# Optimization experiments

Measured on AMD Instinct MI355X. Metric: run time of the kernel, lower is better.

Reference implementation:

```python
import jax, jax.numpy as jnp
import numpy as np

N_NODES = 50000
N_EDGES = 600000
D = 128
R = 8
EPS = 1e-5


def layer_norm(x, g, b):
    mu = jnp.mean(x, axis=-1, keepdims=True)
    var = jnp.mean(jnp.square(x - mu), axis=-1, keepdims=True)
    return (x - mu) * jax.lax.rsqrt(var + EPS) * g + b


def rgcn(x, src, dst, edge_attr, W, root, bias, num_nodes):
    # x: [N, d], W: [R, d, f], edge_attr: [E, R] soft relation weights
    E = src.shape[0]
    f = W.shape[-1]
    msg = jnp.zeros((E, f), dtype=x.dtype)
    for r in range(W.shape[0]):  # small fixed relation count
        hr = x @ W[r]                       # [N, f]
        msg = msg + hr[src] * edge_attr[:, r][:, None]  # gather + weight
    agg = jax.ops.segment_sum(msg, dst, num_segments=num_nodes)  # scatter-add
    return agg + x @ root + bias


def setup_inputs() -> dict:
    key = jax.random.key(0)
    ks = jax.random.split(key, 12)
    s = 1.0 / np.sqrt(D)
    return {
        "x": jax.random.normal(ks[0], (N_NODES, D), dtype=jnp.float32),
        "edge_index": jax.random.randint(ks[1], (2, N_EDGES), 0, N_NODES, dtype=jnp.int64),
        "edge_attr": jax.random.uniform(ks[2], (N_EDGES, R), dtype=jnp.float32),
        "ln1_g": jnp.ones((D,), jnp.float32),
        "ln1_b": jnp.zeros((D,), jnp.float32),
        "W1": jax.random.normal(ks[3], (R, D, D), jnp.float32) * s,
        "root1": jax.random.normal(ks[4], (D, D), jnp.float32) * s,
        "b1": jnp.zeros((D,), jnp.float32),
        "ln2_g": jnp.ones((D,), jnp.float32),
        "ln2_b": jnp.zeros((D,), jnp.float32),
        "W2": jax.random.normal(ks[5], (R, D, D), jnp.float32) * s,
        "root2": jax.random.normal(ks[6], (D, D), jnp.float32) * s,
        "b2": jnp.zeros((D,), jnp.float32),
    }


def reference(x, edge_index, edge_attr, ln1_g, ln1_b, W1, root1, b1,
              ln2_g, ln2_b, W2, root2, b2):
    src, dst = edge_index[0], edge_index[1]
    identity = x
    out = jax.nn.gelu(layer_norm(x, ln1_g, ln1_b), approximate=False)
    out = rgcn(out, src, dst, edge_attr, W1, root1, b1, x.shape[0])
    out = jax.nn.gelu(layer_norm(out, ln2_g, ln2_b), approximate=False)
    out = rgcn(out, src, dst, edge_attr, W2, root2, b2, x.shape[0])
    return out + identity
```

## Files before the change

### kernel.cpp

```cpp
#include <hip/hip_runtime.h>
#include <hip/hip_bf16.h>

typedef __attribute__((ext_vector_type(8))) short short8;
typedef __attribute__((ext_vector_type(4))) float f32x4;

#define LDA 1152

__device__ __forceinline__ float bf2f(unsigned short u) {
    union { unsigned int i; float f; } v; v.i = ((unsigned int)u) << 16; return v.f;
}
__device__ __forceinline__ unsigned short f2bf(float f) {
    __hip_bfloat16 h = __float2bfloat16(f);
    union { __hip_bfloat16 h; unsigned short u; } v; v.h = h; return v.u;
}
__device__ __forceinline__ float gelu_exact(float t) {
    return 0.5f * t * (1.0f + erff(t * 0.70710678118654752f));
}

__global__ void prep_w(const float* __restrict__ W1, const float* __restrict__ root1,
                       unsigned short* __restrict__ Bf1,
                       const float* __restrict__ W2, const float* __restrict__ root2,
                       unsigned short* __restrict__ Bf2) {
    int i = blockIdx.x * 256 + threadIdx.x;
    const float* W = W1; const float* root = root1; unsigned short* Bfrag = Bf1;
    if (i >= 1152 * 128) {
        i -= 1152 * 128; W = W2; root = root2; Bfrag = Bf2;
        if (i >= 1152 * 128) return;
    }
    int kp = i >> 7, n = i & 127;
    float v;
    if (kp < 1024) {
        int d = kp >> 3, r = kp & 7;
        v = W[((size_t)r * 128 + d) * 128 + n];
    } else {
        v = root[(size_t)(kp - 1024) * 128 + n];
    }
    int kb = kp >> 5;
    int lane = (((kp >> 3) & 3) << 4) | (n & 15);
    int j = kp & 7;
    int t = n >> 4;
    Bfrag[(((size_t)(kb * 8 + t) * 64 + lane) << 3) + j] = f2bf(v);
}

__global__ void zero_i32(int* __restrict__ p, int n) {
    int i = blockIdx.x * 256 + threadIdx.x;
    if (i < n) p[i] = 0;
}

__global__ void hist_dst(const int* __restrict__ ei, int* __restrict__ cnt, int E) {
    int e = blockIdx.x * 256 + threadIdx.x;
    if (e >= E) return;
    atomicAdd(&cnt[ei[E + e]], 1);
}

__global__ void scan1(const int* __restrict__ cnt, int* __restrict__ part,
                      int* __restrict__ bsum, int N) {
    int i = blockIdx.x * 256 + threadIdx.x;
    int v = (i < N) ? cnt[i] : 0;
    int lane = threadIdx.x & 63, wid = threadIdx.x >> 6;
    int s = v;
    #pragma unroll
    for (int off = 1; off < 64; off <<= 1) {
        int t = __shfl_up(s, off);
        if (lane >= off) s += t;
    }
    __shared__ int wsum[4];
    if (lane == 63) wsum[wid] = s;
    __syncthreads();
    int add = 0;
    for (int w = 0; w < wid; ++w) add += wsum[w];
    s += add;
    part[i] = s - v;
    if (threadIdx.x == 255) bsum[blockIdx.x] = s;
}

__global__ void scan2(int* __restrict__ bsum, int nb) {
    int i = threadIdx.x;
    int v = (i < nb) ? bsum[i] : 0;
    int lane = threadIdx.x & 63, wid = threadIdx.x >> 6;
    int s = v;
    #pragma unroll
    for (int off = 1; off < 64; off <<= 1) {
        int t = __shfl_up(s, off);
        if (lane >= off) s += t;
    }
    __shared__ int wsum[4];
    if (lane == 63) wsum[wid] = s;
    __syncthreads();
    int add = 0;
    for (int w = 0; w < wid; ++w) add += wsum[w];
    s += add;
    if (i < nb) bsum[i] = s - v;
}

__global__ void scan3(const int* __restrict__ part, const int* __restrict__ bsum,
                      int* __restrict__ rowptr, int* __restrict__ woff, int N) {
    int i = blockIdx.x * 256 + threadIdx.x;
    if (i >= N) return;
    int v = part[i] + bsum[blockIdx.x];
    rowptr[i] = v;
    woff[i] = v;
}

__global__ void scatter_edges(const int* __restrict__ ei, const float4* __restrict__ attr,
                              int* __restrict__ woff, int* __restrict__ esrc,
                              float4* __restrict__ eattr, int E) {
    int e = blockIdx.x * 256 + threadIdx.x;
    if (e >= E) return;
    int src = ei[e], dst = ei[E + e];
    int p = atomicAdd(&woff[dst], 1);
    esrc[p] = src;
    eattr[2 * p]     = attr[2 * e];
    eattr[2 * p + 1] = attr[2 * e + 1];
}

__global__ void ln_gelu(const float* __restrict__ x, const float* __restrict__ g,
                        const float* __restrict__ b, unsigned short* __restrict__ A, int N) {
    int row = (blockIdx.x * blockDim.x + threadIdx.x) >> 6;
    if (row >= N) return;
    int lane = threadIdx.x & 63;
    float2 v = *(const float2*)(x + (size_t)row * 128 + lane * 2);
    float s = v.x + v.y;
    #pragma unroll
    for (int o = 32; o; o >>= 1) s += __shfl_xor(s, o);
    float mu = s * (1.0f / 128.0f);
    float d0 = v.x - mu, d1 = v.y - mu;
    float q = d0 * d0 + d1 * d1;
    #pragma unroll
    for (int o = 32; o; o >>= 1) q += __shfl_xor(q, o);
    float rs = rsqrtf(q * (1.0f / 128.0f) + 1e-5f);
    float2 gg = *(const float2*)(g + lane * 2);
    float2 bb = *(const float2*)(b + lane * 2);
    ushort2 o2;
    o2.x = f2bf(gelu_exact(d0 * rs * gg.x + bb.x));
    o2.y = f2bf(gelu_exact(d1 * rs * gg.y + bb.y));
    *(ushort2*)(A + (size_t)row * LDA + 1024 + lane * 2) = o2;
}

__global__ __launch_bounds__(256) void edge_z(const int* __restrict__ rowptr,
                                              const int* __restrict__ esrc,
                                              const float4* __restrict__ eattr,
                                              unsigned short* __restrict__ A, int N, int E) {
    int row = (blockIdx.x << 2) + (threadIdx.x >> 6);
    if (row >= N) return;
    int lane = threadIdx.x & 63;
    int e0 = rowptr[row];
    int e1 = (row + 1 < N) ? rowptr[row + 1] : E;
    float a0[8] = {0,0,0,0,0,0,0,0};
    float a1[8] = {0,0,0,0,0,0,0,0};
    const unsigned short* yl = A + 1024 + lane * 2;

    #define EDGE_FMA(hv, W0, W1) do {                                  \
        float y0 = bf2f((unsigned short)((hv) & 0xffffu));             \
        float y1 = bf2f((unsigned short)((hv) >> 16));                 \
        a0[0] += (W0).x * y0; a1[0] += (W0).x * y1;                    \
        a0[1] += (W0).y * y0; a1[1] += (W0).y * y1;                    \
        a0[2] += (W0).z * y0; a1[2] += (W0).z * y1;                    \
        a0[3] += (W0).w * y0; a1[3] += (W0).w * y1;                    \
        a0[4] += (W1).x * y0; a1[4] += (W1).x * y1;                    \
        a0[5] += (W1).y * y0; a1[5] += (W1).y * y1;                    \
        a0[6] += (W1).z * y0; a1[6] += (W1).z * y1;                    \
        a0[7] += (W1).w * y0; a1[7] += (W1).w * y1;                    \
    } while (0)

    int e = e0;
    for (; e + 8 <= e1; e += 8) {
        unsigned int h[8];
        #pragma unroll
        for (int u = 0; u < 8; ++u)
            h[u] = *(const unsigned int*)(yl + (size_t)esrc[e + u] * LDA);
        #pragma unroll
        for (int u = 0; u < 8; ++u) {
            float4 w0 = eattr[2 * (e + u)], w1 = eattr[2 * (e + u) + 1];
            EDGE_FMA(h[u], w0, w1);
        }
    }
    for (; e + 4 <= e1; e += 4) {
        unsigned int h[4];
        #pragma unroll
        for (int u = 0; u < 4; ++u)
            h[u] = *(const unsigned int*)(yl + (size_t)esrc[e + u] * LDA);
        #pragma unroll
        for (int u = 0; u < 4; ++u) {
            float4 w0 = eattr[2 * (e + u)], w1 = eattr[2 * (e + u) + 1];
            EDGE_FMA(h[u], w0, w1);
        }
    }
    for (; e < e1; ++e) {
        unsigned int h = *(const unsigned int*)(yl + (size_t)esrc[e] * LDA);
        float4 w0 = eattr[2 * e], w1 = eattr[2 * e + 1];
        EDGE_FMA(h, w0, w1);
    }
    #undef EDGE_FMA

    short8 p0, p1;
    #pragma unroll
    for (int r = 0; r < 8; ++r) { p0[r] = (short)f2bf(a0[r]); p1[r] = (short)f2bf(a1[r]); }
    unsigned short* zr = A + (size_t)row * LDA + lane * 16;
    *(short8*)zr = p0;
    *(short8*)(zr + 8) = p1;
}

template <int MODE>
__global__ __launch_bounds__(256) void gemm_fused(
        unsigned short* __restrict__ A, const unsigned short* __restrict__ Bfrag,
        const float* __restrict__ bias, const float* __restrict__ lng,
        const float* __restrict__ lnb, const float* __restrict__ xres,
        float* __restrict__ outp, int N) {
    int gw = (blockIdx.x * 256 + threadIdx.x) >> 6;
    int lane = threadIdx.x & 63;
    int l15 = lane & 15, lhi = lane >> 4;
    int m0 = gw * 32;

    const unsigned short* a0p = A + (size_t)(m0 + l15) * LDA + lhi * 8;
    const unsigned short* a1p = a0p + 16 * LDA;
    const short8* bfb = (const short8*)Bfrag + lane;

    short8 bA[8], bB[8];
    #pragma unroll
    for (int t = 0; t < 8; ++t) bA[t] = bfb[t * 64];
    short8 aA0 = *(const short8*)a0p;
    short8 aA1 = *(const short8*)a1p;

    f32x4 acc0[8] = {}, acc1[8] = {};
    for (int kb = 0; kb < 36; kb += 2) {
        #pragma unroll
        for (int t = 0; t < 8; ++t) bB[t] = bfb[((kb + 1) * 8 + t) * 64];
        short8 aB0 = *(const short8*)(a0p + (kb + 1) * 32);
        short8 aB1 = *(const short8*)(a1p + (kb + 1) * 32);
        #pragma unroll
        for (int t = 0; t < 8; ++t) {
            acc0[t] = __builtin_amdgcn_mfma_f32_16x16x32_bf16(aA0, bA[t], acc0[t], 0, 0, 0);
            acc1[t] = __builtin_amdgcn_mfma_f32_16x16x32_bf16(aA1, bA[t], acc1[t], 0, 0, 0);
        }
        if (kb + 2 < 36) {
            #pragma unroll
            for (int t = 0; t < 8; ++t) bA[t] = bfb[((kb + 2) * 8 + t) * 64];
            aA0 = *(const short8*)(a0p + (kb + 2) * 32);
            aA1 = *(const short8*)(a1p + (kb + 2) * 32);
        }
        #pragma unroll
        for (int t = 0; t < 8; ++t) {
            acc0[t] = __builtin_amdgcn_mfma_f32_16x16x32_bf16(aB0, bB[t], acc0[t], 0, 0, 0);
            acc1[t] = __builtin_amdgcn_mfma_f32_16x16x32_bf16(aB1, bB[t], acc1[t], 0, 0, 0);
        }
    }

    float bcol[8];
    #pragma unroll
    for (int t = 0; t < 8; ++t) bcol[t] = bias[t * 16 + l15];

    if (MODE == 0) {
        float gcol[8], lbcol[8];
        #pragma unroll
        for (int t = 0; t < 8; ++t) { gcol[t] = lng[t * 16 + l15]; lbcol[t] = lnb[t * 16 + l15]; }
        #pragma unroll
        for (int g = 0; g < 2; ++g) {
            int mb = m0 + g * 16;
            #pragma unroll
            for (int reg = 0; reg < 4; ++reg) {
                int row = mb + lhi * 4 + reg;
                float tv[8];
                float s = 0.f;
                #pragma unroll
                for (int t = 0; t < 8; ++t) {
                    tv[t] = (g ? acc1[t][reg] : acc0[t][reg]) + bcol[t];
                    s += tv[t];
                }
                #pragma unroll
                for (int msk = 1; msk < 16; msk <<= 1) s += __shfl_xor(s, msk);
                float mu = s * (1.0f / 128.0f);
                float q = 0.f;
                #pragma unroll
                for (int t = 0; t < 8; ++t) { float d = tv[t] - mu; q += d * d; }
                #pragma unroll
                for (int msk = 1; msk < 16; msk <<= 1) q += __shfl_xor(q, msk);
                float rs = rsqrtf(q * (1.0f / 128.0f) + 1e-5f);
                if (row < N) {
                    #pragma unroll
                    for (int t = 0; t < 8; ++t) {
                        float u = gelu_exact((tv[t] - mu) * rs * gcol[t] + lbcol[t]);
                        A[(size_t)row * LDA + 1024 + t * 16 + l15] = f2bf(u);
                    }
                }
            }
        }
    } else {
        #pragma unroll
        for (int g = 0; g < 2; ++g) {
            int mb = m0 + g * 16;
            #pragma unroll
            for (int reg = 0; reg < 4; ++reg) {
                int row = mb + lhi * 4 + reg;
                if (row < N) {
                    #pragma unroll
                    for (int t = 0; t < 8; ++t) {
                        size_t idx = (size_t)row * 128 + t * 16 + l15;
                        outp[idx] = (g ? acc1[t][reg] : acc0[t][reg]) + bcol[t] + xres[idx];
                    }
                }
            }
        }
    }
}

extern "C" void kernel_launch(void* const* d_in, const int* in_sizes, int n_in,
                              void* d_out, int out_size, void* d_ws, size_t ws_size,
                              hipStream_t stream) {
    const float* x     = (const float*)d_in[0];
    const int*   ei    = (const int*)d_in[1];
    const float* attr  = (const float*)d_in[2];
    const float* ln1g  = (const float*)d_in[3];
    const float* ln1b  = (const float*)d_in[4];
    const float* W1    = (const float*)d_in[5];
    const float* root1 = (const float*)d_in[6];
    const float* b1    = (const float*)d_in[7];
    const float* ln2g  = (const float*)d_in[8];
    const float* ln2b  = (const float*)d_in[9];
    const float* W2    = (const float*)d_in[10];
    const float* root2 = (const float*)d_in[11];
    const float* b2    = (const float*)d_in[12];

    const int N = in_sizes[0] / 128;
    const int E = in_sizes[1] / 2;

    char* ws = (char*)d_ws;
    unsigned short* A     = (unsigned short*)(ws);
    unsigned short* Bf1   = (unsigned short*)(ws + 115400000);
    unsigned short* Bf2   = (unsigned short*)(ws + 115700000);
    int*            cnt   = (int*)(ws + 116000000);
    int*            part  = (int*)(ws + 116210000);
    int*            bsum  = (int*)(ws + 116420000);
    int*            rowptr= (int*)(ws + 116430000);
    int*            woff  = (int*)(ws + 116640000);
    int*            esrc  = (int*)(ws + 116850000);
    float4*         eattr = (float4*)(ws + 119250000);

    const int scanBlocks  = (N + 255) / 256;
    const int edgeBlocksE = (E + 255) / 256;
    const int rowsBlocks  = (N * 64 + 255) / 256;
    const int nodeBlocks  = (N + 3) / 4;
    const int gemmBlocks  = (N + 127) / 128;

    prep_w<<<1152, 256, 0, stream>>>(W1, root1, Bf1, W2, root2, Bf2);

    zero_i32<<<scanBlocks, 256, 0, stream>>>(cnt, scanBlocks * 256);
    hist_dst<<<edgeBlocksE, 256, 0, stream>>>(ei, cnt, E);
    scan1<<<scanBlocks, 256, 0, stream>>>(cnt, part, bsum, N);
    scan2<<<1, 256, 0, stream>>>(bsum, scanBlocks);
    scan3<<<scanBlocks, 256, 0, stream>>>(part, bsum, rowptr, woff, N);
    scatter_edges<<<edgeBlocksE, 256, 0, stream>>>(ei, (const float4*)attr, woff, esrc, eattr, E);

    ln_gelu<<<rowsBlocks, 256, 0, stream>>>(x, ln1g, ln1b, A, N);
    edge_z<<<nodeBlocks, 256, 0, stream>>>(rowptr, esrc, eattr, A, N, E);
    gemm_fused<0><<<gemmBlocks, 256, 0, stream>>>(A, Bf1, b1, ln2g, ln2b, nullptr, nullptr, N);

    edge_z<<<nodeBlocks, 256, 0, stream>>>(rowptr, esrc, eattr, A, N, E);
    gemm_fused<1><<<gemmBlocks, 256, 0, stream>>>(A, Bf2, b2, nullptr, nullptr, x, (float*)d_out, N);
}
```

Baseline: 302.2 us.

## Stage GEMM weights through LDS with double buffering and pack edge attrs as bf16

The GEMM now uses 512-thread blocks covering 256 rows and stages weight fragments into double-buffered shared memory with global_load_lds, so all eight waves share each weight load instead of each wave reading it from global memory. A fragments are prefetched in chunks of four k-steps with a sync per chunk. Edge attributes are converted to bf16 and packed into 16 bytes per edge at scatter time, which halves the per-edge attribute traffic in edge_z at the cost of reduced weight precision. The 8-wide edge unroll is dropped in favour of a 4-wide loop. Workspace offsets are shifted, and the A buffer now has to be padded to a multiple of 256 rows.

```diff
diff --git a/kernel.cpp b/kernel.cpp
--- a/kernel.cpp
+++ b/kernel.cpp
@@ -104,14 +104,19 @@
 
 __global__ void scatter_edges(const int* __restrict__ ei, const float4* __restrict__ attr,
                               int* __restrict__ woff, int* __restrict__ esrc,
-                              float4* __restrict__ eattr, int E) {
+                              short8* __restrict__ eattr, int E) {
     int e = blockIdx.x * 256 + threadIdx.x;
     if (e >= E) return;
     int src = ei[e], dst = ei[E + e];
+    float4 a0 = attr[2 * e], a1 = attr[2 * e + 1];
+    short8 pk;
+    pk[0] = (short)f2bf(a0.x); pk[1] = (short)f2bf(a0.y);
+    pk[2] = (short)f2bf(a0.z); pk[3] = (short)f2bf(a0.w);
+    pk[4] = (short)f2bf(a1.x); pk[5] = (short)f2bf(a1.y);
+    pk[6] = (short)f2bf(a1.z); pk[7] = (short)f2bf(a1.w);
     int p = atomicAdd(&woff[dst], 1);
     esrc[p] = src;
-    eattr[2 * p]     = attr[2 * e];
-    eattr[2 * p + 1] = attr[2 * e + 1];
+    eattr[p] = pk;
 }
 
 __global__ void ln_gelu(const float* __restrict__ x, const float* __restrict__ g,
@@ -139,7 +144,7 @@
 
 __global__ __launch_bounds__(256) void edge_z(const int* __restrict__ rowptr,
                                               const int* __restrict__ esrc,
-                                              const float4* __restrict__ eattr,
+                                              const short8* __restrict__ eattr,
                                               unsigned short* __restrict__ A, int N, int E) {
     int row = (blockIdx.x << 2) + (threadIdx.x >> 6);
     if (row >= N) return;
@@ -150,46 +155,32 @@
     float a1[8] = {0,0,0,0,0,0,0,0};
     const unsigned short* yl = A + 1024 + lane * 2;
 
-    #define EDGE_FMA(hv, W0, W1) do {                                  \
+    #define EDGE_FMA(hv, ea) do {                                      \
         float y0 = bf2f((unsigned short)((hv) & 0xffffu));             \
         float y1 = bf2f((unsigned short)((hv) >> 16));                 \
-        a0[0] += (W0).x * y0; a1[0] += (W0).x * y1;                    \
-        a0[1] += (W0).y * y0; a1[1] += (W0).y * y1;                    \
-        a0[2] += (W0).z * y0; a1[2] += (W0).z * y1;                    \
-        a0[3] += (W0).w * y0; a1[3] += (W0).w * y1;                    \
-        a0[4] += (W1).x * y0; a1[4] += (W1).x * y1;                    \
-        a0[5] += (W1).y * y0; a1[5] += (W1).y * y1;                    \
-        a0[6] += (W1).z * y0; a1[6] += (W1).z * y1;                    \
-        a0[7] += (W1).w * y0; a1[7] += (W1).w * y1;                    \
+        _Pragma("unroll")                                              \
+        for (int r = 0; r < 8; ++r) {                                  \
+            float wv = bf2f((unsigned short)(ea)[r]);                  \
+            a0[r] += wv * y0; a1[r] += wv * y1;                        \
+        }                                                              \
     } while (0)
 
     int e = e0;
-    for (; e + 8 <= e1; e += 8) {
-        unsigned int h[8];
-        #pragma unroll
-        for (int u = 0; u < 8; ++u)
-            h[u] = *(const unsigned int*)(yl + (size_t)esrc[e + u] * LDA);
-        #pragma unroll
-        for (int u = 0; u < 8; ++u) {
-            float4 w0 = eattr[2 * (e + u)], w1 = eattr[2 * (e + u) + 1];
-            EDGE_FMA(h[u], w0, w1);
-        }
-    }
     for (; e + 4 <= e1; e += 4) {
         unsigned int h[4];
-        #pragma unroll
-        for (int u = 0; u < 4; ++u)
+        short8 ea[4];
+        #pragma unroll
+        for (int u = 0; u < 4; ++u) {
             h[u] = *(const unsigned int*)(yl + (size_t)esrc[e + u] * LDA);
-        #pragma unroll
-        for (int u = 0; u < 4; ++u) {
-            float4 w0 = eattr[2 * (e + u)], w1 = eattr[2 * (e + u) + 1];
-            EDGE_FMA(h[u], w0, w1);
-        }
+            ea[u] = eattr[e + u];
+        }
+        #pragma unroll
+        for (int u = 0; u < 4; ++u) EDGE_FMA(h[u], ea[u]);
     }
     for (; e < e1; ++e) {
         unsigned int h = *(const unsigned int*)(yl + (size_t)esrc[e] * LDA);
-        float4 w0 = eattr[2 * e], w1 = eattr[2 * e + 1];
-        EDGE_FMA(h, w0, w1);
+        short8 ea = eattr[e];
+        EDGE_FMA(h, ea);
     }
     #undef EDGE_FMA
 
@@ -202,49 +193,63 @@
 }
 
 template <int MODE>
-__global__ __launch_bounds__(256) void gemm_fused(
+__global__ __launch_bounds__(512) void gemm_fused(
         unsigned short* __restrict__ A, const unsigned short* __restrict__ Bfrag,
         const float* __restrict__ bias, const float* __restrict__ lng,
         const float* __restrict__ lnb, const float* __restrict__ xres,
         float* __restrict__ outp, int N) {
-    int gw = (blockIdx.x * 256 + threadIdx.x) >> 6;
+    __shared__ short8 Bs[2][2048];
+
+    int w = threadIdx.x >> 6;
     int lane = threadIdx.x & 63;
     int l15 = lane & 15, lhi = lane >> 4;
-    int m0 = gw * 32;
+    int m0 = blockIdx.x * 256 + w * 32;
 
     const unsigned short* a0p = A + (size_t)(m0 + l15) * LDA + lhi * 8;
     const unsigned short* a1p = a0p + 16 * LDA;
-    const short8* bfb = (const short8*)Bfrag + lane;
-
-    short8 bA[8], bB[8];
-    #pragma unroll
-    for (int t = 0; t < 8; ++t) bA[t] = bfb[t * 64];
-    short8 aA0 = *(const short8*)a0p;
-    short8 aA1 = *(const short8*)a1p;
+    const short8* bfb = (const short8*)Bfrag;
+
+    #define STAGE(buf, c)                                                          \
+        do {                                                                       \
+            const short8* gsrc = bfb + (size_t)(c) * 2048 + w * 64;                \
+            _Pragma("unroll")                                                      \
+            for (int i = 0; i < 4; ++i)                                            \
+                __builtin_amdgcn_global_load_lds(&gsrc[i * 512 + lane],            \
+                                                 &Bs[buf][w * 64 + i * 512], 16, 0, 0); \
+        } while (0)
+
+    STAGE(0, 0);
+    short8 af0[4], af1[4];
+    #pragma unroll
+    for (int k = 0; k < 4; ++k) {
+        af0[k] = *(const short8*)(a0p + k * 32);
+        af1[k] = *(const short8*)(a1p + k * 32);
+    }
+    __syncthreads();
 
     f32x4 acc0[8] = {}, acc1[8] = {};
-    for (int kb = 0; kb < 36; kb += 2) {
-        #pragma unroll
-        for (int t = 0; t < 8; ++t) bB[t] = bfb[((kb + 1) * 8 + t) * 64];
-        short8 aB0 = *(const short8*)(a0p + (kb + 1) * 32);
-        short8 aB1 = *(const short8*)(a1p + (kb + 1) * 32);
-        #pragma unroll
-        for (int t = 0; t < 8; ++t) {
-            acc0[t] = __builtin_amdgcn_mfma_f32_16x16x32_bf16(aA0, bA[t], acc0[t], 0, 0, 0);
-            acc1[t] = __builtin_amdgcn_mfma_f32_16x16x32_bf16(aA1, bA[t], acc1[t], 0, 0, 0);
-        }
-        if (kb + 2 < 36) {
+    for (int c = 0; c < 9; ++c) {
+        int cur = c & 1;
+        if (c < 8) STAGE(cur ^ 1, c + 1);
+        #pragma unroll
+        for (int k = 0; k < 4; ++k) {
             #pragma unroll
-            for (int t = 0; t < 8; ++t) bA[t] = bfb[((kb + 2) * 8 + t) * 64];
-            aA0 = *(const short8*)(a0p + (kb + 2) * 32);
-            aA1 = *(const short8*)(a1p + (kb + 2) * 32);
-        }
-        #pragma unroll
-        for (int t = 0; t < 8; ++t) {
-            acc0[t] = __builtin_amdgcn_mfma_f32_16x16x32_bf16(aB0, bB[t], acc0[t], 0, 0, 0);
-            acc1[t] = __builtin_amdgcn_mfma_f32_16x16x32_bf16(aB1, bB[t], acc1[t], 0, 0, 0);
-        }
-    }
+            for (int t = 0; t < 8; ++t) {
+                short8 b = Bs[cur][k * 512 + t * 64 + lane];
+                acc0[t] = __builtin_amdgcn_mfma_f32_16x16x32_bf16(af0[k], b, acc0[t], 0, 0, 0);
+                acc1[t] = __builtin_amdgcn_mfma_f32_16x16x32_bf16(af1[k], b, acc1[t], 0, 0, 0);
+            }
+        }
+        if (c < 8) {
+            #pragma unroll
+            for (int k = 0; k < 4; ++k) {
+                af0[k] = *(const short8*)(a0p + ((c + 1) * 4 + k) * 32);
+                af1[k] = *(const short8*)(a1p + ((c + 1) * 4 + k) * 32);
+            }
+            __syncthreads();
+        }
+    }
+    #undef STAGE
 
     float bcol[8];
     #pragma unroll
@@ -326,21 +331,21 @@
 
     char* ws = (char*)d_ws;
     unsigned short* A     = (unsigned short*)(ws);
-    unsigned short* Bf1   = (unsigned short*)(ws + 115400000);
-    unsigned short* Bf2   = (unsigned short*)(ws + 115700000);
-    int*            cnt   = (int*)(ws + 116000000);
-    int*            part  = (int*)(ws + 116210000);
-    int*            bsum  = (int*)(ws + 116420000);
-    int*            rowptr= (int*)(ws + 116430000);
-    int*            woff  = (int*)(ws + 116640000);
-    int*            esrc  = (int*)(ws + 116850000);
-    float4*         eattr = (float4*)(ws + 119250000);
+    unsigned short* Bf1   = (unsigned short*)(ws + 115700000);
+    unsigned short* Bf2   = (unsigned short*)(ws + 116000000);
+    int*            cnt   = (int*)(ws + 116300000);
+    int*            part  = (int*)(ws + 116510000);
+    int*            bsum  = (int*)(ws + 116720000);
+    int*            rowptr= (int*)(ws + 116730000);
+    int*            woff  = (int*)(ws + 116940000);
+    int*            esrc  = (int*)(ws + 117150000);
+    short8*         eattr = (short8*)(ws + 119560000);
 
     const int scanBlocks  = (N + 255) / 256;
     const int edgeBlocksE = (E + 255) / 256;
     const int rowsBlocks  = (N * 64 + 255) / 256;
     const int nodeBlocks  = (N + 3) / 4;
-    const int gemmBlocks  = (N + 127) / 128;
+    const int gemmBlocks  = (N + 255) / 256;
 
     prep_w<<<1152, 256, 0, stream>>>(W1, root1, Bf1, W2, root2, Bf2);
 
@@ -353,8 +358,8 @@
 
     ln_gelu<<<rowsBlocks, 256, 0, stream>>>(x, ln1g, ln1b, A, N);
     edge_z<<<nodeBlocks, 256, 0, stream>>>(rowptr, esrc, eattr, A, N, E);
-    gemm_fused<0><<<gemmBlocks, 256, 0, stream>>>(A, Bf1, b1, ln2g, ln2b, nullptr, nullptr, N);
+    gemm_fused<0><<<gemmBlocks, 512, 0, stream>>>(A, Bf1, b1, ln2g, ln2b, nullptr, nullptr, N);
 
     edge_z<<<nodeBlocks, 256, 0, stream>>>(rowptr, esrc, eattr, A, N, E);
-    gemm_fused<1><<<gemmBlocks, 256, 0, stream>>>(A, Bf2, b2, nullptr, nullptr, x, (float*)d_out, N);
-}
+    gemm_fused<1><<<gemmBlocks, 512, 0, stream>>>(A, Bf2, b2, nullptr, nullptr, x, (float*)d_out, N);
+}
```

After: 258.2 us. 14.6% less time.
